# Kernel tuning notes

Measured on AMD Instinct MI355X. Metric: run time of the kernel, lower is better.

## Reference

```python
import jax, jax.numpy as jnp
from jax import lax
import numpy as np

B = 2
N_PER = 12000
TIMES = 16
C_IN = 4
# sparse_shape = grid_size[::-1] + [1,0,0], grid_size=[160,160,40]
S1 = (41, 160, 160)
S2 = (21, 80, 80)   # conv2: k3 s2 p1
S3 = (11, 40, 40)   # conv3: k3 s2 p1
S4 = (5, 20, 20)    # conv4: k3 s2 p(0,1,1)
SOUT = (2, 20, 20)  # conv_out: k(3,1,1) s(2,1,1) p0
# per-BN-layer channel counts, flattened into gamma/beta vectors
CH = [16, 16, 32, 32, 32, 64, 64, 64, 64, 64, 64, 128]
OFF = np.concatenate([[0], np.cumsum(CH)]).tolist()


def _downsample_coords(coords, in_shape, k, s, p):
    # spconv SparseConv3d output index rule: output j active iff some active
    # input x satisfies j*s - p <= x <= j*s - p + k - 1 within bounds.
    out_shape = np.array([(in_shape[i] + 2 * p[i] - k[i]) // s[i] + 1 for i in range(3)])
    b, xs = coords[:, :1], coords[:, 1:]
    s_arr = np.array(s)
    cand = []
    for o0 in range(k[0]):
        for o1 in range(k[1]):
            for o2 in range(k[2]):
                j = xs + np.array([p[0] - o0, p[1] - o1, p[2] - o2])
                ok = np.all(j % s_arr == 0, axis=1)
                jj = j // s_arr
                ok &= np.all((jj >= 0) & (jj < out_shape), axis=1)
                cand.append(np.concatenate([b[ok], jj[ok]], axis=1))
    return np.unique(np.concatenate(cand, axis=0), axis=0).astype(np.int32)


def _make_coords():
    rng = np.random.default_rng(0)
    ncell = S1[0] * S1[1] * S1[2]
    per = []
    for b in range(B):
        flat = rng.choice(ncell, size=N_PER, replace=False)
        z, y, x = np.unravel_index(flat, S1)
        per.append(np.stack([np.full(N_PER, b), z, y, x], axis=1))
    c1 = np.concatenate(per, axis=0).astype(np.int32)
    c2 = _downsample_coords(c1, S1, (3, 3, 3), (2, 2, 2), (1, 1, 1))
    c3 = _downsample_coords(c2, S2, (3, 3, 3), (2, 2, 2), (1, 1, 1))
    c4 = _downsample_coords(c3, S3, (3, 3, 3), (2, 2, 2), (0, 1, 1))
    c5 = _downsample_coords(c4, S4, (3, 1, 1), (2, 1, 1), (0, 0, 0))
    return c1, c2, c3, c4, c5


def _w(key, shape):
    fan_in = shape[0] * shape[1] * shape[2] * shape[3]
    return jax.random.normal(key, shape, jnp.float32) * np.float32(np.sqrt(2.0 / fan_in))


def setup_inputs():
    c1, c2, c3, c4, c5 = _make_coords()
    ks = jax.random.split(jax.random.key(0), 16)
    t = TIMES
    return {
        "voxel_features": jax.random.normal(ks[0], (c1.shape[0], C_IN), jnp.float32),
        "w_in": _w(ks[1], (3, 3, 3, C_IN, t)),
        "w1": _w(ks[2], (3, 3, 3, t, t)),
        "w2_0": _w(ks[3], (3, 3, 3, t, 2 * t)),
        "w2_1": _w(ks[4], (3, 3, 3, 2 * t, 2 * t)),
        "w2_2": _w(ks[5], (3, 3, 3, 2 * t, 2 * t)),
        "w3_0": _w(ks[6], (3, 3, 3, 2 * t, 4 * t)),
        "w3_1": _w(ks[7], (3, 3, 3, 4 * t, 4 * t)),
        "w3_2": _w(ks[8], (3, 3, 3, 4 * t, 4 * t)),
        "w4_0": _w(ks[9], (3, 3, 3, 4 * t, 4 * t)),
        "w4_1": _w(ks[10], (3, 3, 3, 4 * t, 4 * t)),
        "w4_2": _w(ks[11], (3, 3, 3, 4 * t, 4 * t)),
        "w_out": _w(ks[12], (3, 1, 1, 4 * t, 8 * t)),
        "gamma": 1.0 + 0.1 * jax.random.normal(ks[13], (sum(CH),), jnp.float32),
        "beta": 0.1 * jax.random.normal(ks[14], (sum(CH),), jnp.float32),
        "coords1": jnp.asarray(c1), "coords2": jnp.asarray(c2),
        "coords3": jnp.asarray(c3), "coords4": jnp.asarray(c4),
        "coords_out": jnp.asarray(c5),
    }


def _sp_conv(feats, in_coords, w, in_shape, out_coords, stride, padding):
    # spconv's rulebook gather->matmul->scatter over active sites computes the
    # same values as a dense conv on a zero-filled grid, read back only at the
    # active output coordinates (subm: out_coords == in_coords).
    dense = jnp.zeros((B,) + in_shape + (feats.shape[1],), feats.dtype)
    dense = dense.at[in_coords[:, 0], in_coords[:, 1], in_coords[:, 2], in_coords[:, 3]].set(feats)
    out = lax.conv_general_dilated(dense, w, window_strides=stride,
                                   padding=[(p, p) for p in padding],
                                   dimension_numbers=("NDHWC", "DHWIO", "NDHWC"))
    return out[out_coords[:, 0], out_coords[:, 1], out_coords[:, 2], out_coords[:, 3]]


def _bn_relu(x, g, b):
    # nn.BatchNorm1d(eps=1e-3) in training mode over the active voxels, + ReLU
    mu = jnp.mean(x, axis=0)
    var = jnp.mean(jnp.square(x - mu), axis=0)
    return jax.nn.relu((x - mu) * (g * lax.rsqrt(var + 1e-3)) + b)


def _forward(voxel_features, ws, gamma, beta, c1, c2, c3, c4, c5):
    layers = [
        (0, c1, S1, c1, (1, 1, 1), (1, 1, 1)),   # conv_input (subm, 4->16)
        (1, c1, S1, c1, (1, 1, 1), (1, 1, 1)),   # conv1 (subm)
        (2, c1, S1, c2, (2, 2, 2), (1, 1, 1)),   # conv2 spconv s2
        (3, c2, S2, c2, (1, 1, 1), (1, 1, 1)),
        (4, c2, S2, c2, (1, 1, 1), (1, 1, 1)),
        (5, c2, S2, c3, (2, 2, 2), (1, 1, 1)),   # conv3 spconv s2
        (6, c3, S3, c3, (1, 1, 1), (1, 1, 1)),
        (7, c3, S3, c3, (1, 1, 1), (1, 1, 1)),
        (8, c3, S3, c4, (2, 2, 2), (0, 1, 1)),   # conv4 spconv s2, pad (0,1,1)
        (9, c4, S4, c4, (1, 1, 1), (1, 1, 1)),
        (10, c4, S4, c4, (1, 1, 1), (1, 1, 1)),
        (11, c4, S4, c5, (2, 1, 1), (0, 0, 0)),  # conv_out k(3,1,1) s(2,1,1)
    ]
    x = voxel_features
    for i, ci, si, co, st, pd in layers:
        x = _sp_conv(x, ci, ws[i], si, co, st, pd)
        x = _bn_relu(x, gamma[OFF[i]:OFF[i + 1]], beta[OFF[i]:OFF[i + 1]])
    return x  # encoded_spconv_tensor features, [N_out, 8*times]


def reference(voxel_features, w_in, w1, w2_0, w2_1, w2_2, w3_0, w3_1, w3_2,
              w4_0, w4_1, w4_2, w_out, gamma, beta,
              coords1, coords2, coords3, coords4, coords_out):
    ws = [w_in, w1, w2_0, w2_1, w2_2, w3_0, w3_1, w3_2, w4_0, w4_1, w4_2, w_out]
    return _forward(voxel_features, ws, gamma, beta,
                    coords1, coords2, coords3, coords4, coords_out)
```

## Files before the change

### kernel.cpp

```cpp
#include <hip/hip_runtime.h>
#include <hip/hip_bf16.h>


typedef __attribute__((ext_vector_type(8))) short bf16x8;
typedef __attribute__((ext_vector_type(4))) short bf16x4s;
typedef __attribute__((ext_vector_type(4))) float f32x4;

typedef const __attribute__((address_space(1))) unsigned int* gas_ptr;
typedef __attribute__((address_space(3))) unsigned int* las_ptr;

__device__ __forceinline__ void dma16(const unsigned short* g, unsigned short* l) {
    __builtin_amdgcn_global_load_lds((gas_ptr)g, (las_ptr)l, 16, 0, 0);
}

__device__ inline unsigned short f2bf(float f) {
    unsigned u = __builtin_bit_cast(unsigned, f);
    u += 0x7FFFu + ((u >> 16) & 1u);
    return (unsigned short)(u >> 16);
}

struct ScatterArgs {
    const int* coords[4];
    int* grid[4];
    int n[4];
    int D[4], H[4], W[4];
};

__global__ __launch_bounds__(256) void scatter_grid_all(ScatterArgs a) {
    const int l = blockIdx.y;
    const int i = blockIdx.x * 256 + threadIdx.x;
    if (i >= a.n[l]) return;
    const int* c = a.coords[l] + 4 * i;
    a.grid[l][((c[0] * a.D[l] + c[1]) * a.H[l] + c[2]) * a.W[l] + c[3]] = i;
}

struct PrepArgs {
    const float* src[11];
    unsigned short* dst[11];
    int T[11], CIN[11], COUT[11], total[11];
};

__global__ __launch_bounds__(256) void prep_w_all(PrepArgs a) {
    const int l = blockIdx.y;
    const int i = blockIdx.x * 256 + threadIdx.x;
    if (i >= a.total[l]) return;
    const int COUT = a.COUT[l], CIN = a.CIN[l], T = a.T[l];
    const int co = i % COUT; const int r = i / COUT; const int ci = r % CIN; const int t = r / CIN;
    unsigned short v = (t < T) ? f2bf(a.src[l][i]) : (unsigned short)0;
    a.dst[l][((size_t)t * COUT + co) * CIN + ci] = v;
}

__global__ __launch_bounds__(256, 4) void sp_conv0(const float* __restrict__ fin,
                                                   const int* __restrict__ grid,
                                                   const int* __restrict__ oc, int n_out,
                                                   const float* __restrict__ w,
                                                   float* __restrict__ out,
                                                   int D, int H, int W) {
    const int c = threadIdx.x & 15;
    const int p = (blockIdx.x * 256 + threadIdx.x) >> 4;
    if (p >= n_out) return;
    const int b   = oc[4*p+0];
    const int iz0 = oc[4*p+1] - 1;
    const int iy0 = oc[4*p+2] - 1;
    const int ix0 = oc[4*p+3] - 1;
    const int* gb = grid + b * (D * H * W);
    float acc = 0.f;
    for (int kd = 0; kd < 3; ++kd) {
        const int iz = iz0 + kd;
        if ((unsigned)iz >= (unsigned)D) continue;
        for (int kh = 0; kh < 3; ++kh) {
            const int iy = iy0 + kh;
            if ((unsigned)iy >= (unsigned)H) continue;
            for (int kw = 0; kw < 3; ++kw) {
                const int ix = ix0 + kw;
                if ((unsigned)ix >= (unsigned)W) continue;
                const int idx = gb[(iz*H + iy)*W + ix];
                if (idx < 0) continue;
                const float4 v = *(const float4*)(fin + (size_t)idx * 4);
                const float* wp = w + (size_t)((kd*3 + kh)*3 + kw) * 64 + c;
                acc = fmaf(v.x, wp[0],  acc);
                acc = fmaf(v.y, wp[16], acc);
                acc = fmaf(v.z, wp[32], acc);
                acc = fmaf(v.w, wp[48], acc);
            }
        }
    }
    out[(size_t)p*16 + c] = acc;
}

template<int COUT, int BT>
__global__ __launch_bounds__(256, 4) void sp_conv_lds16(
    const unsigned short* __restrict__ fin, const int* __restrict__ grid,
    const int* __restrict__ oc, int n_out,
    const unsigned short* __restrict__ wt, float* __restrict__ out,
    float* __restrict__ stats,
    int D, int H, int W, int sz, int sy, int sx, int pz, int py, int px)
{
    constexpr int T  = 27;
    constexpr int NBATCH = (T + BT - 1)/BT;
    constexpr int TP = NBATCH*BT;
    constexpr int NT = COUT/16;
    constexpr int NB = (COUT == 16) ? BT/2 : BT;

    __shared__ unsigned short Abuf[4*BT*16*16];
    __shared__ unsigned short Bbuf[BT*COUT*16];
    __shared__ float ls[2*COUT];

    const int l     = threadIdx.x & 63;
    const int w     = threadIdx.x >> 6;
    const int n     = l & 15;
    const int quad  = l >> 4;
    const int pbase = blockIdx.x * 64 + w * 16;

    if (threadIdx.x < 2*COUT) ls[threadIdx.x] = 0.f;

    int idx[TP];
    if (quad == 0) {
        int pc = pbase + n;
        if (pc > n_out - 1) pc = n_out - 1;
        const int4 cc = ((const int4*)oc)[pc];
        const int* gb = grid + cc.x * (D * H * W);
        const int iz0 = cc.y * sz - pz;
        const int iy0 = cc.z * sy - py;
        const int ix0 = cc.w * sx - px;
#pragma unroll
        for (int tap = 0; tap < TP; ++tap) {
            const int te = tap < T ? tap : 0;
            const int kd = te/9, kr = te%9, kh = kr/3, kw = kr%3;
            const int iz = iz0 + kd, iy = iy0 + kh, ix = ix0 + kw;
            const bool ok = (tap < T) && (unsigned)iz < (unsigned)D &&
                            (unsigned)iy < (unsigned)H && (unsigned)ix < (unsigned)W;
            const int cz = iz < 0 ? 0 : (iz >= D ? D-1 : iz);
            const int cy = iy < 0 ? 0 : (iy >= H ? H-1 : iy);
            const int cx = ix < 0 ? 0 : (ix >= W ? W-1 : ix);
            const int g = gb[(cz*H + cy)*W + cx];
            idx[tap] = ok ? g : -1;
        }
    }

    f32x4 acc[NT];
#pragma unroll
    for (int t = 0; t < NT; ++t) acc[t] = (f32x4){0.f, 0.f, 0.f, 0.f};

    const int h  = l >> 5;
    const int m  = (l >> 1) & 15;
    const int ch = l & 1;

#pragma unroll
    for (int tb0 = 0; tb0 < TP; tb0 += BT) {
#pragma unroll
        for (int q = 0; q < BT/2; ++q) {
            const int v0 = __shfl(idx[tb0 + 2*q],     m);
            const int v1 = __shfl(idx[tb0 + 2*q + 1], m);
            const int row = h ? v1 : v0;
            const unsigned short* gp = fin + (ptrdiff_t)row*16 + ch*8;
            unsigned short* lp = Abuf + (w*BT + 2*q)*16*16;
            dma16(gp, lp);
        }
        for (int q = w; q < NB; q += 4) {
            if constexpr (COUT == 16) {
                const int tap = tb0 + 2*q + h;
                const int tw = tap < T ? tap : T;
                const unsigned short* gp = wt + ((size_t)tw*COUT + m)*16 + ch*8;
                unsigned short* lp = Bbuf + (2*q)*COUT*16;
                dma16(gp, lp);
            } else {
                const int tap = tb0 + q;
                const int tw = tap < T ? tap : T;
                const int r = l >> 1;
                const unsigned short* gp = wt + ((size_t)tw*COUT + r)*16 + ch*8;
                unsigned short* lp = Bbuf + q*COUT*16;
                dma16(gp, lp);
            }
        }
        __syncthreads();
#pragma unroll
        for (int jp = 0; jp < BT/2; ++jp) {
            const int ts = 2*jp + (quad >> 1);
            bf16x8 a = *(const bf16x8*)(Abuf + ((w*BT + ts)*16 + n)*16 + (quad & 1)*8);
#pragma unroll
            for (int t = 0; t < NT; ++t) {
                bf16x8 b = *(const bf16x8*)(Bbuf + (ts*COUT + t*16 + n)*16 + (quad & 1)*8);
                acc[t] = __builtin_amdgcn_mfma_f32_16x16x32_bf16(a, b, acc[t], 0, 0, 0);
            }
        }
        __syncthreads();
    }

#pragma unroll
    for (int t = 0; t < NT; ++t)
#pragma unroll
        for (int r = 0; r < 4; ++r) {
            const int p = pbase + quad*4 + r;
            if (p < n_out) out[(size_t)p * COUT + t*16 + n] = acc[t][r];
        }

#pragma unroll
    for (int t = 0; t < NT; ++t) {
        float s1 = 0.f, s2 = 0.f;
#pragma unroll
        for (int r = 0; r < 4; ++r) {
            const int p = pbase + quad*4 + r;
            if (p < n_out) { const float v = acc[t][r]; s1 += v; s2 += v*v; }
        }
        s1 += __shfl_xor(s1, 16); s2 += __shfl_xor(s2, 16);
        s1 += __shfl_xor(s1, 32); s2 += __shfl_xor(s2, 32);
        if (quad == 0) {
            atomicAdd(&ls[t*16 + n], s1);
            atomicAdd(&ls[COUT + t*16 + n], s2);
        }
    }
    __syncthreads();
    if (threadIdx.x < 2*COUT) atomicAdd(&stats[threadIdx.x], ls[threadIdx.x]);
}

template<int CIN, int COUT, int BT, int KD, int KH, int KW, int MB>
__global__ __launch_bounds__(256, MB) void sp_conv_lds(
    const unsigned short* __restrict__ fin, const int* __restrict__ grid,
    const int* __restrict__ oc, int n_out,
    const unsigned short* __restrict__ wt, float* __restrict__ out,
    float* __restrict__ stats,
    int D, int H, int W, int sz, int sy, int sx, int pz, int py, int px)
{
    constexpr int T    = KD*KH*KW;
    constexpr int NBATCH = (T + BT - 1)/BT;
    constexpr int TP   = NBATCH*BT;
    constexpr int NT   = COUT/16;
    constexpr int S    = CIN/32;
    constexpr int LPR  = CIN/8;
    constexpr int RPD  = 64/LPR;
    constexpr int ADMA = 16/RPD;
    constexpr int BDMA = COUT/RPD;

    __shared__ unsigned short Abuf[4*BT*16*CIN];
    __shared__ unsigned short Bbuf[BT*COUT*CIN];
    __shared__ float ls[2*COUT];

    const int l     = threadIdx.x & 63;
    const int w     = threadIdx.x >> 6;
    const int n     = l & 15;
    const int quad  = l >> 4;
    const int pbase = blockIdx.x * 64 + w * 16;

    if (threadIdx.x < 2*COUT) ls[threadIdx.x] = 0.f;

    int idx[TP];
    if (quad == 0) {
        int pc = pbase + n;
        if (pc > n_out - 1) pc = n_out - 1;
        const int4 cc = ((const int4*)oc)[pc];
        const int* gb = grid + cc.x * (D * H * W);
        const int iz0 = cc.y * sz - pz;
        const int iy0 = cc.z * sy - py;
        const int ix0 = cc.w * sx - px;
#pragma unroll
        for (int tap = 0; tap < TP; ++tap) {
            const int te = tap < T ? tap : 0;
            const int kd = te/(KH*KW), kr = te%(KH*KW), kh = kr/KW, kw = kr%KW;
            const int iz = iz0 + kd, iy = iy0 + kh, ix = ix0 + kw;
            const bool ok = (tap < T) && (unsigned)iz < (unsigned)D &&
                            (unsigned)iy < (unsigned)H && (unsigned)ix < (unsigned)W;
            const int cz = iz < 0 ? 0 : (iz >= D ? D-1 : iz);
            const int cy = iy < 0 ? 0 : (iy >= H ? H-1 : iy);
            const int cx = ix < 0 ? 0 : (ix >= W ? W-1 : ix);
            const int g = gb[(cz*H + cy)*W + cx];
            idx[tap] = ok ? g : -1;
        }
    }

    f32x4 acc[NT];
#pragma unroll
    for (int t = 0; t < NT; ++t) acc[t] = (f32x4){0.f, 0.f, 0.f, 0.f};

#pragma unroll
    for (int tb0 = 0; tb0 < TP; tb0 += BT) {
#pragma unroll
        for (int j = 0; j < BT; ++j) {
#pragma unroll
            for (int d = 0; d < ADMA; ++d) {
                const int m  = d*RPD + l/LPR;
                const int i0 = __shfl(idx[tb0+j], m);
                const int slot = (l % LPR) ^ (m % LPR);
                const unsigned short* gp = fin + (ptrdiff_t)i0*CIN + slot*8;
                unsigned short* lp = Abuf + ((w*BT + j)*16 + d*RPD)*CIN;
                dma16(gp, lp);
            }
        }
        for (int q = w; q < BT*BDMA; q += 4) {
            const int j = q / BDMA, d = q % BDMA;
            const int t = tb0 + j;
            const int tw = t < T ? t : T;
            const int r  = d*RPD + l/LPR;
            const int slot = (l % LPR) ^ (r % LPR);
            const unsigned short* gp = wt + ((size_t)tw*COUT + r)*CIN + slot*8;
            unsigned short* lp = Bbuf + (j*COUT + d*RPD)*CIN;
            dma16(gp, lp);
        }
        __syncthreads();
#pragma unroll
        for (int j = 0; j < BT; ++j) {
            const unsigned short* Aw = Abuf + (w*BT + j)*16*CIN;
            const unsigned short* Bw = Bbuf + j*COUT*CIN;
#pragma unroll
            for (int s = 0; s < S; ++s) {
                const int c = s*4 + quad;
                bf16x8 a = *(const bf16x8*)(Aw + n*CIN + ((c ^ (n % LPR)) * 8));
#pragma unroll
                for (int t = 0; t < NT; ++t) {
                    const int r = t*16 + n;
                    bf16x8 b = *(const bf16x8*)(Bw + r*CIN + ((c ^ (r % LPR)) * 8));
                    acc[t] = __builtin_amdgcn_mfma_f32_16x16x32_bf16(a, b, acc[t], 0, 0, 0);
                }
            }
        }
        __syncthreads();
    }

#pragma unroll
    for (int t = 0; t < NT; ++t)
#pragma unroll
        for (int r = 0; r < 4; ++r) {
            const int p = pbase + quad*4 + r;
            if (p < n_out) out[(size_t)p * COUT + t*16 + n] = acc[t][r];
        }

#pragma unroll
    for (int t = 0; t < NT; ++t) {
        float s1 = 0.f, s2 = 0.f;
#pragma unroll
        for (int r = 0; r < 4; ++r) {
            const int p = pbase + quad*4 + r;
            if (p < n_out) { const float v = acc[t][r]; s1 += v; s2 += v*v; }
        }
        s1 += __shfl_xor(s1, 16); s2 += __shfl_xor(s2, 16);
        s1 += __shfl_xor(s1, 32); s2 += __shfl_xor(s2, 32);
        if (quad == 0) {
            atomicAdd(&ls[t*16 + n], s1);
            atomicAdd(&ls[COUT + t*16 + n], s2);
        }
    }
    __syncthreads();
    if (threadIdx.x < 2*COUT) atomicAdd(&stats[threadIdx.x], ls[threadIdx.x]);
}

template<int C, int TZ, int TY, int TX, int BTW>
__global__ __launch_bounds__(256, 1) void sp_conv_dense(
    const unsigned short* __restrict__ dense, const int* __restrict__ grid,
    const unsigned short* __restrict__ wt, float* __restrict__ out,
    float* __restrict__ stats, const unsigned short* __restrict__ zrow,
    int D, int H, int W, int ZTn, int YTn, int XTn)
{
    constexpr int T   = 27;
    constexpr int HZ = TZ+2, HY = TY+2, HX = TX+2;
    constexpr int R   = HZ*HY*HX;
    constexpr int LPR = C/8;
    constexpr int RPD = 64/LPR;
    constexpr int RPI = 4*RPD;
    constexpr int NDMA = (R + RPI - 1)/RPI;
    constexpr int RPAD = NDMA*RPI;
    constexpr int M   = TZ*TY*TX;
    constexpr int WPW = M/4;
    constexpr int MT  = WPW/16;
    constexpr int NT  = C/16;
    constexpr int S   = C/32;
    constexpr int BDMA = C/RPD;

    __shared__ unsigned short Hbuf[RPAD*C];
    __shared__ unsigned short Bbuf[BTW*C*C];
    __shared__ float ls[2*C];

    const int l    = threadIdx.x & 63;
    const int w    = threadIdx.x >> 6;
    const int n    = l & 15;
    const int quad = l >> 4;

    int r1 = blockIdx.x;
    const int xt = r1 % XTn; r1 /= XTn;
    const int yt = r1 % YTn; r1 /= YTn;
    const int zt = r1 % ZTn; r1 /= ZTn;
    const int b  = r1;
    const int z0 = zt*TZ, y0 = yt*TY, x0 = xt*TX;
    const int* gb = grid + b * (D*H*W);
    const size_t dbase = (size_t)b * D*H*W;

    if (threadIdx.x < 2*C) ls[threadIdx.x] = 0.f;

#pragma unroll
    for (int d = 0; d < NDMA; ++d) {
        const int r0  = (d*4 + w)*RPD;
        const int row = r0 + l/LPR;
        const int slot = (l % LPR) ^ (row % LPR);
        const unsigned short* gp;
        if (row < R) {
            const int hz = row/(HY*HX);
            const int hy = (row/HX) % HY;
            const int hx = row % HX;
            const int gz = z0 - 1 + hz, gy = y0 - 1 + hy, gx = x0 - 1 + hx;
            const bool ok = (unsigned)gz < (unsigned)D && (unsigned)gy < (unsigned)H &&
                            (unsigned)gx < (unsigned)W;
            gp = ok ? dense + (dbase + (size_t)(gz*H + gy)*W + gx)*C + slot*8
                    : zrow + (l % LPR)*8;
        } else {
            gp = zrow + (l % LPR)*8;
        }
        dma16(gp, Hbuf + r0*C);
    }

    int prow[MT];
#pragma unroll
    for (int mt = 0; mt < MT; ++mt) {
        const int pos = w*WPW + mt*16 + n;
        const int dz = pos/(TY*TX), dy = (pos/TX)%TY, dx = pos%TX;
        prow[mt] = dz*(HY*HX) + dy*HX + dx;
    }

    f32x4 acc[MT][NT];
#pragma unroll
    for (int mt = 0; mt < MT; ++mt)
#pragma unroll
        for (int t = 0; t < NT; ++t) acc[mt][t] = (f32x4){0.f, 0.f, 0.f, 0.f};

#pragma unroll
    for (int batch = 0; batch < (T + BTW - 1)/BTW; ++batch) {
        const int tb0 = batch*BTW;
        const int nb  = (tb0 + BTW <= T) ? BTW : T - tb0;
        for (int q = w; q < nb*BDMA; q += 4) {
            const int j = q / BDMA, d = q % BDMA;
            const int tap = tb0 + j;
            const int rr  = d*RPD + l/LPR;
            const int slot = (l % LPR) ^ (rr % LPR);
            dma16(wt + ((size_t)tap*C + rr)*C + slot*8, Bbuf + (j*C + d*RPD)*C);
        }
        __syncthreads();
#pragma unroll
        for (int j = 0; j < nb; ++j) {
            const int tap = tb0 + j;
            const int kd = tap/9, kh = (tap/3)%3, kw = tap%3;
            const int toff = kd*(HY*HX) + kh*HX + kw;
#pragma unroll
            for (int s = 0; s < S; ++s) {
                const int c = s*4 + quad;
                bf16x8 bfr[NT];
#pragma unroll
                for (int t = 0; t < NT; ++t) {
                    const int rr = t*16 + n;
                    bfr[t] = *(const bf16x8*)(Bbuf + (j*C + rr)*C + ((c ^ (rr & (LPR-1)))*8));
                }
#pragma unroll
                for (int mt = 0; mt < MT; ++mt) {
                    const int arow = prow[mt] + toff;
                    bf16x8 a = *(const bf16x8*)(Hbuf + arow*C + ((c ^ (arow & (LPR-1)))*8));
#pragma unroll
                    for (int t = 0; t < NT; ++t)
                        acc[mt][t] = __builtin_amdgcn_mfma_f32_16x16x32_bf16(a, bfr[t], acc[mt][t], 0, 0, 0);
                }
            }
        }
        __syncthreads();
    }

    float s1[NT], s2[NT];
#pragma unroll
    for (int t = 0; t < NT; ++t) { s1[t] = 0.f; s2[t] = 0.f; }
#pragma unroll
    for (int mt = 0; mt < MT; ++mt) {
#pragma unroll
        for (int r = 0; r < 4; ++r) {
            const int pos = w*WPW + mt*16 + quad*4 + r;
            const int dz = pos/(TY*TX), dy = (pos/TX)%TY, dx = pos%TX;
            const int gz = z0 + dz, gy = y0 + dy, gx = x0 + dx;
            int p = -1;
            if (gz < D && gy < H && gx < W) p = gb[(gz*H + gy)*W + gx];
            if (p >= 0) {
#pragma unroll
                for (int t = 0; t < NT; ++t) {
                    const float v = acc[mt][t][r];
                    out[(size_t)p*C + t*16 + n] = v;
                    s1[t] += v; s2[t] += v*v;
                }
            }
        }
    }
#pragma unroll
    for (int t = 0; t < NT; ++t) {
        float a1 = s1[t], a2 = s2[t];
        a1 += __shfl_xor(a1, 16); a2 += __shfl_xor(a2, 16);
        a1 += __shfl_xor(a1, 32); a2 += __shfl_xor(a2, 32);
        if (quad == 0) {
            atomicAdd(&ls[t*16 + n], a1);
            atomicAdd(&ls[C + t*16 + n], a2);
        }
    }
    __syncthreads();
    if (threadIdx.x < 2*C) atomicAdd(&stats[threadIdx.x], ls[threadIdx.x]);
}

template<int C>
__global__ __launch_bounds__(256) void reduce_stats(const float* __restrict__ x, int nn,
                                                    float* __restrict__ stats)
{
    constexpr int R = 256 / C;
    __shared__ float s1[256];
    __shared__ float s2[256];
    const int c = threadIdx.x % C;
    const int r = threadIdx.x / C;
    float a1 = 0.f, a2 = 0.f;
    for (int i = blockIdx.x * R + r; i < nn; i += R * gridDim.x) {
        float v = x[(size_t)i*C + c];
        a1 += v;
        a2 += v * v;
    }
    s1[threadIdx.x] = a1;
    s2[threadIdx.x] = a2;
    __syncthreads();
    for (int off = 128; off >= C; off >>= 1) {
        if (threadIdx.x < off) {
            s1[threadIdx.x] += s1[threadIdx.x + off];
            s2[threadIdx.x] += s2[threadIdx.x + off];
        }
        __syncthreads();
    }
    if (threadIdx.x < C) {
        atomicAdd(&stats[c],     s1[threadIdx.x]);
        atomicAdd(&stats[C + c], s2[threadIdx.x]);
    }
}

__device__ inline void stv4(float* p, float4 v) { *(float4*)p = v; }
__device__ inline void stv4(unsigned short* p, float4 v) {
    bf16x4s o;
    o.x = (short)f2bf(v.x); o.y = (short)f2bf(v.y);
    o.z = (short)f2bf(v.z); o.w = (short)f2bf(v.w);
    *(bf16x4s*)p = o;
}

__device__ inline float4 bn_math(float4 xv, float4 s1, float4 s2, float4 gm, float4 bt,
                                 float inv_n) {
    float4 o;
    { float mu=s1.x*inv_n, var=s2.x*inv_n-mu*mu, g=gm.x*rsqrtf(var+1e-3f);
      float v=(xv.x-mu)*g+bt.x; o.x = v>0.f? v:0.f; }
    { float mu=s1.y*inv_n, var=s2.y*inv_n-mu*mu, g=gm.y*rsqrtf(var+1e-3f);
      float v=(xv.y-mu)*g+bt.y; o.y = v>0.f? v:0.f; }
    { float mu=s1.z*inv_n, var=s2.z*inv_n-mu*mu, g=gm.z*rsqrtf(var+1e-3f);
      float v=(xv.z-mu)*g+bt.z; o.z = v>0.f? v:0.f; }
    { float mu=s1.w*inv_n, var=s2.w*inv_n-mu*mu, g=gm.w*rsqrtf(var+1e-3f);
      float v=(xv.w-mu)*g+bt.w; o.w = v>0.f? v:0.f; }
    return o;
}

template<int C, typename OUT>
__global__ __launch_bounds__(256) void bn_relu_apply(const float* __restrict__ x,
                                                     OUT* __restrict__ y, int nn,
                                                     const float* __restrict__ stats,
                                                     const float* __restrict__ gamma,
                                                     const float* __restrict__ beta)
{
    const size_t q = (size_t)blockIdx.x * blockDim.x + threadIdx.x;
    if (q >= (size_t)nn * (C/4)) return;
    const int c = (int)(q % (size_t)(C/4)) * 4;
    const float4 o = bn_math(*(const float4*)(x + q*4),
                             *(const float4*)(stats + c), *(const float4*)(stats + C + c),
                             *(const float4*)(gamma + c), *(const float4*)(beta + c),
                             1.f / (float)nn);
    stv4(y + q*4, o);
}

template<int C>
__global__ __launch_bounds__(256) void bn_relu_apply_dense(const float* __restrict__ x,
                                                           unsigned short* __restrict__ dense,
                                                           int nn,
                                                           const float* __restrict__ stats,
                                                           const float* __restrict__ gamma,
                                                           const float* __restrict__ beta,
                                                           const int* __restrict__ coords,
                                                           int D, int H, int W)
{
    const size_t q = (size_t)blockIdx.x * blockDim.x + threadIdx.x;
    if (q >= (size_t)nn * (C/4)) return;
    const int c = (int)(q % (size_t)(C/4)) * 4;
    const int p = (int)(q / (size_t)(C/4));
    const float4 o = bn_math(*(const float4*)(x + q*4),
                             *(const float4*)(stats + c), *(const float4*)(stats + C + c),
                             *(const float4*)(gamma + c), *(const float4*)(beta + c),
                             1.f / (float)nn);
    const int4 cc = ((const int4*)coords)[p];
    const size_t cell = ((size_t)((cc.x*D + cc.y)*H + cc.z)*W + cc.w);
    stv4(dense + cell*C + c, o);
}

extern "C" void kernel_launch(void* const* d_in, const int* in_sizes, int n_in,
                              void* d_out, int out_size, void* d_ws, size_t ws_size,
                              hipStream_t stream) {
    const float* WPTR[12] = {
        (const float*)d_in[1], (const float*)d_in[2], (const float*)d_in[3],
        (const float*)d_in[4], (const float*)d_in[5], (const float*)d_in[6],
        (const float*)d_in[7], (const float*)d_in[8], (const float*)d_in[9],
        (const float*)d_in[10], (const float*)d_in[11], (const float*)d_in[12] };
    const float* vf    = (const float*)d_in[0];
    const float* gamma = (const float*)d_in[13];
    const float* beta  = (const float*)d_in[14];
    const int* c1 = (const int*)d_in[15];
    const int* c2 = (const int*)d_in[16];
    const int* c3 = (const int*)d_in[17];
    const int* c4 = (const int*)d_in[18];
    const int* c5 = (const int*)d_in[19];
    const int N1 = in_sizes[15] / 4;
    const int N2 = in_sizes[16] / 4;
    const int N3 = in_sizes[17] / 4;
    const int N4 = in_sizes[18] / 4;
    const int N5 = in_sizes[19] / 4;

    static const int LT[12]  = {27,27,27,27,27,27,27,27,27,27,27,3};
    static const int LCI[12] = {4,16,16,32,32,32,64,64,64,64,64,64};
    static const int LCO[12] = {16,16,32,32,32,64,64,64,64,64,64,128};

    const size_t G1 = (size_t)2*41*160*160;
    const size_t G2 = (size_t)2*21*80*80;
    const size_t G3 = (size_t)2*11*40*40;
    const size_t G4 = (size_t)2*5*20*20;
    int* grid1 = (int*)d_ws;
    int* grid2 = grid1 + G1;
    int* grid3 = grid2 + G2;
    int* grid4 = grid3 + G3;
    float* stats = (float*)(grid4 + G4);

    size_t maxE = (size_t)N1*16;
    if ((size_t)N2*32  > maxE) maxE = (size_t)N2*32;
    if ((size_t)N3*64  > maxE) maxE = (size_t)N3*64;
    if ((size_t)N4*64  > maxE) maxE = (size_t)N4*64;
    if ((size_t)N5*128 > maxE) maxE = (size_t)N5*128;
    maxE = (maxE + 7) & ~(size_t)7;

    float* raw = stats + 12*256;
    unsigned short* padA = (unsigned short*)(raw + maxE);
    unsigned short* fA   = padA + 128;
    unsigned short* padB = fA + maxE;
    unsigned short* fB   = padB + 128;
    unsigned short* wtb  = fB + maxE;
    size_t wtoff[12];
    size_t wtot = 0;
    {
        size_t o = 0;
        for (int i = 1; i < 12; ++i) {
            wtoff[i] = o;
            o += (size_t)(LT[i] + 1) * LCI[i] * LCO[i];
        }
        wtot = (o + 15) & ~(size_t)15;
    }
    unsigned short* dbuf = wtb + wtot;

    hipMemsetAsync(grid1, 0xFF, (G1+G2+G3+G4)*sizeof(int), stream);
    hipMemsetAsync(stats, 0, 12*256*sizeof(float), stream);
    hipMemsetAsync(padA, 0, 128*sizeof(unsigned short), stream);
    hipMemsetAsync(padB, 0, 128*sizeof(unsigned short), stream);

    {
        ScatterArgs sa;
        sa.coords[0]=c1; sa.coords[1]=c2; sa.coords[2]=c3; sa.coords[3]=c4;
        sa.grid[0]=grid1; sa.grid[1]=grid2; sa.grid[2]=grid3; sa.grid[3]=grid4;
        sa.n[0]=N1; sa.n[1]=N2; sa.n[2]=N3; sa.n[3]=N4;
        sa.D[0]=41; sa.H[0]=160; sa.W[0]=160;
        sa.D[1]=21; sa.H[1]= 80; sa.W[1]= 80;
        sa.D[2]=11; sa.H[2]= 40; sa.W[2]= 40;
        sa.D[3]= 5; sa.H[3]= 20; sa.W[3]= 20;
        int mx = N1; if (N2>mx) mx=N2; if (N3>mx) mx=N3; if (N4>mx) mx=N4;
        dim3 g((mx + 255)/256, 4);
        scatter_grid_all<<<g, 256, 0, stream>>>(sa);
    }
    {
        PrepArgs pa;
        int mx = 0;
        for (int i = 1; i < 12; ++i) {
            pa.src[i-1] = WPTR[i];
            pa.dst[i-1] = wtb + wtoff[i];
            pa.T[i-1] = LT[i]; pa.CIN[i-1] = LCI[i]; pa.COUT[i-1] = LCO[i];
            pa.total[i-1] = (LT[i]+1)*LCI[i]*LCO[i];
            if (pa.total[i-1] > mx) mx = pa.total[i-1];
        }
        dim3 g((mx + 255)/256, 11);
        prep_w_all<<<g, 256, 0, stream>>>(pa);
    }

    enum { GOFF_0 = 0, GOFF_1 = 16, GOFF_2 = 32, GOFF_3 = 64, GOFF_4 = 96, GOFF_5 = 128,
           GOFF_6 = 192, GOFF_7 = 256, GOFF_8 = 320, GOFF_9 = 384, GOFF_10 = 448, GOFF_11 = 512 };

#define APPLY(i, COUT, NP, FOUT_T, FOUT) \
    bn_relu_apply<COUT, FOUT_T><<<(((size_t)(NP)*(COUT)/4) + 255)/256, 256, 0, stream>>>( \
        raw, FOUT, NP, stats + (i)*256, gamma + GOFF_##i, beta + GOFF_##i);

#define APPLYD(i, C, NP, CC, D,H,W) \
    hipMemsetAsync(dbuf, 0, (size_t)2*(D)*(H)*(W)*(C)*2, stream); \
    bn_relu_apply_dense<C><<<(((size_t)(NP)*(C)/4) + 255)/256, 256, 0, stream>>>( \
        raw, dbuf, NP, stats + (i)*256, gamma + GOFF_##i, beta + GOFF_##i, CC, D,H,W);

    sp_conv0<<<((size_t)N1*16 + 255)/256, 256, 0, stream>>>(vf, grid1, c1, N1, WPTR[0], raw, 41,160,160);
    { int rb = (N1 + 15)/16; if (rb > 240) rb = 240;
      reduce_stats<16><<<rb, 256, 0, stream>>>(raw, N1, stats + 0*256); }
    APPLY(0, 16, N1, unsigned short, fA);

#define CONVS(i, COUT, BT, FIN, GRD, OC, NP, D,H,W, SZ,SY,SX, PZ,PY,PX) \
    sp_conv_lds16<COUT,BT><<<((NP)+63)/64, 256, 0, stream>>>( \
        FIN, GRD, OC, NP, wtb + wtoff[i], raw, stats + (i)*256, D,H,W, SZ,SY,SX, PZ,PY,PX);

#define CONVL(i, CIN, COUT, BT, MB, KD,KH,KW, FIN, GRD, OC, NP, D,H,W, SZ,SY,SX, PZ,PY,PX) \
    sp_conv_lds<CIN,COUT,BT,KD,KH,KW,MB><<<((NP)+63)/64, 256, 0, stream>>>( \
        FIN, GRD, OC, NP, wtb + wtoff[i], raw, stats + (i)*256, D,H,W, SZ,SY,SX, PZ,PY,PX);

#define CONVD(i, C, TZ,TY,TX, BTW, GRD, D,H,W) \
    { const int zt = ((D)+(TZ)-1)/(TZ), yt = ((H)+(TY)-1)/(TY), xt = ((W)+(TX)-1)/(TX); \
      sp_conv_dense<C,TZ,TY,TX,BTW><<<2*zt*yt*xt, 256, 0, stream>>>( \
          dbuf, GRD, wtb + wtoff[i], raw, stats + (i)*256, padA, D,H,W, zt,yt,xt); }

    CONVS( 1, 16, 10,   fA, grid1, c1, N1, 41,160,160, 1,1,1, 1,1,1); APPLY( 1, 16, N1, unsigned short, fB);
    CONVS( 2, 32, 10,   fB, grid1, c2, N2, 41,160,160, 2,2,2, 1,1,1); APPLYD( 2, 32, N2, c2, 21,80,80);
    CONVD( 3, 32, 4,8,16, 27, grid2, 21,80,80);                       APPLYD( 3, 32, N2, c2, 21,80,80);
    CONVD( 4, 32, 4,8,16, 27, grid2, 21,80,80);                       APPLY( 4, 32, N2, unsigned short, fA);
    CONVL( 5, 32, 64, 9, 2, 3,3,3, fA, grid2, c3, N3, 21,80,80, 2,2,2, 1,1,1); APPLYD( 5, 64, N3, c3, 11,40,40);
    CONVD( 6, 64, 4,4,8, 10, grid3, 11,40,40);                        APPLYD( 6, 64, N3, c3, 11,40,40);
    CONVD( 7, 64, 4,4,8, 10, grid3, 11,40,40);                        APPLY( 7, 64, N3, unsigned short, fB);
    CONVL( 8, 64, 64, 9, 1, 3,3,3, fB, grid3, c4, N4, 11,40,40, 2,2,2, 0,1,1); APPLYD( 8, 64, N4, c4, 5,20,20);
    CONVD( 9, 64, 4,4,8, 10, grid4, 5,20,20);                         APPLYD( 9, 64, N4, c4, 5,20,20);
    CONVD(10, 64, 4,4,8, 10, grid4, 5,20,20);                         APPLY(10, 64, N4, unsigned short, fA);
    CONVL(11, 64,128, 3, 2, 3,1,1, fA, grid4, c5, N5,  5,20,20, 2,1,1, 0,0,0); APPLY(11, 128, N5, float, (float*)d_out);
#undef CONVS
#undef CONVL
#undef CONVD
#undef APPLY
#undef APPLYD
}
```

Baseline: 462.7 us.

## Replace dense convs at levels 2 and 4 with gather MFMA kernels, add XCD swizzle

Adds an sp_conv_big gather kernel that computes 32 output rows per wave (two M tiles), so each weight fragment feeds more MFMAs. Layers 3 and 4 now use it instead of the dense-grid conv, and layers 9 and 10 use the sparse gather kernel, which removes the dense scatter and memset at those levels. It also adds an XCD-aware remap of block indices, fixes the lds16 tap batch size at 4, and changes the dense kernel's batch and occupancy settings. The risk is more register pressure and whether gather beats dense at the 80x80 density.

```diff
diff --git a/kernel.cpp b/kernel.cpp
--- a/kernel.cpp
+++ b/kernel.cpp
@@ -11,6 +11,12 @@
 
 __device__ __forceinline__ void dma16(const unsigned short* g, unsigned short* l) {
     __builtin_amdgcn_global_load_lds((gas_ptr)g, (las_ptr)l, 16, 0, 0);
+}
+
+__device__ __forceinline__ int xcd_swz(int wg, int nwg) {
+    const int x = wg & 7, i = wg >> 3;
+    const int q = nwg >> 3, r = nwg & 7;
+    return (x < r ? x * (q + 1) : r * (q + 1) + (x - r) * q) + i;
 }
 
 __device__ inline unsigned short f2bf(float f) {
@@ -88,7 +94,7 @@
     out[(size_t)p*16 + c] = acc;
 }
 
-template<int COUT, int BT>
+template<int COUT>
 __global__ __launch_bounds__(256, 4) void sp_conv_lds16(
     const unsigned short* __restrict__ fin, const int* __restrict__ grid,
     const int* __restrict__ oc, int n_out,
@@ -97,8 +103,8 @@
     int D, int H, int W, int sz, int sy, int sx, int pz, int py, int px)
 {
     constexpr int T  = 27;
-    constexpr int NBATCH = (T + BT - 1)/BT;
-    constexpr int TP = NBATCH*BT;
+    constexpr int BT = 4;
+    constexpr int TP = 28;
     constexpr int NT = COUT/16;
     constexpr int NB = (COUT == 16) ? BT/2 : BT;
 
@@ -110,7 +116,7 @@
     const int w     = threadIdx.x >> 6;
     const int n     = l & 15;
     const int quad  = l >> 4;
-    const int pbase = blockIdx.x * 64 + w * 16;
+    const int pbase = xcd_swz(blockIdx.x, gridDim.x) * 64 + w * 16;
 
     if (threadIdx.x < 2*COUT) ls[threadIdx.x] = 0.f;
 
@@ -223,8 +229,7 @@
     int D, int H, int W, int sz, int sy, int sx, int pz, int py, int px)
 {
     constexpr int T    = KD*KH*KW;
-    constexpr int NBATCH = (T + BT - 1)/BT;
-    constexpr int TP   = NBATCH*BT;
+    constexpr int TP   = ((T + BT - 1)/BT)*BT;
     constexpr int NT   = COUT/16;
     constexpr int S    = CIN/32;
     constexpr int LPR  = CIN/8;
@@ -240,7 +245,7 @@
     const int w     = threadIdx.x >> 6;
     const int n     = l & 15;
     const int quad  = l >> 4;
-    const int pbase = blockIdx.x * 64 + w * 16;
+    const int pbase = xcd_swz(blockIdx.x, gridDim.x) * 64 + w * 16;
 
     if (threadIdx.x < 2*COUT) ls[threadIdx.x] = 0.f;
 
@@ -343,8 +348,149 @@
     if (threadIdx.x < 2*COUT) atomicAdd(&stats[threadIdx.x], ls[threadIdx.x]);
 }
 
-template<int C, int TZ, int TY, int TX, int BTW>
-__global__ __launch_bounds__(256, 1) void sp_conv_dense(
+template<int CIN, int COUT, int BT, int MB>
+__global__ __launch_bounds__(256, MB) void sp_conv_big(
+    const unsigned short* __restrict__ fin, const int* __restrict__ grid,
+    const int* __restrict__ oc, int n_out,
+    const unsigned short* __restrict__ wt, float* __restrict__ out,
+    float* __restrict__ stats,
+    int D, int H, int W, int sz, int sy, int sx, int pz, int py, int px)
+{
+    constexpr int T    = 27;
+    constexpr int TP   = 28;
+    constexpr int MT   = 2;
+    constexpr int NT   = COUT/16;
+    constexpr int S    = CIN/32;
+    constexpr int LPR  = CIN/8;
+    constexpr int RPD  = 64/LPR;
+    constexpr int ADMA = 32/RPD;
+    constexpr int BDMA = COUT/RPD;
+
+    __shared__ unsigned short Abuf[4*BT*32*CIN];
+    __shared__ unsigned short Bbuf[BT*COUT*CIN];
+    __shared__ float ls[2*COUT];
+
+    const int l     = threadIdx.x & 63;
+    const int w     = threadIdx.x >> 6;
+    const int n     = l & 15;
+    const int quad  = l >> 4;
+    const int wbase = xcd_swz(blockIdx.x, gridDim.x) * 128 + w * 32;
+
+    if (threadIdx.x < 2*COUT) ls[threadIdx.x] = 0.f;
+
+    int idx[TP];
+    {
+        int pc = wbase + (l & 31);
+        if (pc > n_out - 1) pc = n_out - 1;
+        const int4 cc = ((const int4*)oc)[pc];
+        const int* gb = grid + cc.x * (D * H * W);
+        const int iz0 = cc.y * sz - pz;
+        const int iy0 = cc.z * sy - py;
+        const int ix0 = cc.w * sx - px;
+#pragma unroll
+        for (int tap = 0; tap < TP; ++tap) {
+            const int te = tap < T ? tap : 0;
+            const int kd = te/9, kr = te%9, kh = kr/3, kw = kr%3;
+            const int iz = iz0 + kd, iy = iy0 + kh, ix = ix0 + kw;
+            const bool ok = (tap < T) && (unsigned)iz < (unsigned)D &&
+                            (unsigned)iy < (unsigned)H && (unsigned)ix < (unsigned)W;
+            const int cz = iz < 0 ? 0 : (iz >= D ? D-1 : iz);
+            const int cy = iy < 0 ? 0 : (iy >= H ? H-1 : iy);
+            const int cx = ix < 0 ? 0 : (ix >= W ? W-1 : ix);
+            const int g = gb[(cz*H + cy)*W + cx];
+            idx[tap] = ok ? g : -1;
+        }
+    }
+
+    f32x4 acc[MT][NT];
+#pragma unroll
+    for (int mt = 0; mt < MT; ++mt)
+#pragma unroll
+        for (int t = 0; t < NT; ++t) acc[mt][t] = (f32x4){0.f, 0.f, 0.f, 0.f};
+
+#pragma unroll
+    for (int tb0 = 0; tb0 < TP; tb0 += BT) {
+#pragma unroll
+        for (int j = 0; j < BT; ++j) {
+#pragma unroll
+            for (int d = 0; d < ADMA; ++d) {
+                const int r  = d*RPD + l/LPR;
+                const int i0 = __shfl(idx[tb0+j], r);
+                const int slot = (l % LPR) ^ (r % LPR);
+                const unsigned short* gp = fin + (ptrdiff_t)i0*CIN + slot*8;
+                unsigned short* lp = Abuf + ((w*BT + j)*32 + d*RPD)*CIN;
+                dma16(gp, lp);
+            }
+        }
+        for (int q = w; q < BT*BDMA; q += 4) {
+            const int j = q / BDMA, d = q % BDMA;
+            const int t = tb0 + j;
+            const int tw = t < T ? t : T;
+            const int r  = d*RPD + l/LPR;
+            const int slot = (l % LPR) ^ (r % LPR);
+            const unsigned short* gp = wt + ((size_t)tw*COUT + r)*CIN + slot*8;
+            unsigned short* lp = Bbuf + (j*COUT + d*RPD)*CIN;
+            dma16(gp, lp);
+        }
+        __syncthreads();
+#pragma unroll
+        for (int j = 0; j < BT; ++j) {
+            const unsigned short* Aw = Abuf + (w*BT + j)*32*CIN;
+            const unsigned short* Bw = Bbuf + j*COUT*CIN;
+#pragma unroll
+            for (int s = 0; s < S; ++s) {
+                const int c = s*4 + quad;
+                bf16x8 bfr[NT];
+#pragma unroll
+                for (int t = 0; t < NT; ++t) {
+                    const int r = t*16 + n;
+                    bfr[t] = *(const bf16x8*)(Bw + r*CIN + ((c ^ (r % LPR)) * 8));
+                }
+#pragma unroll
+                for (int mt = 0; mt < MT; ++mt) {
+                    bf16x8 a = *(const bf16x8*)(Aw + (mt*16 + n)*CIN + ((c ^ (n % LPR)) * 8));
+#pragma unroll
+                    for (int t = 0; t < NT; ++t)
+                        acc[mt][t] = __builtin_amdgcn_mfma_f32_16x16x32_bf16(a, bfr[t], acc[mt][t], 0, 0, 0);
+                }
+            }
+        }
+        __syncthreads();
+    }
+
+#pragma unroll
+    for (int mt = 0; mt < MT; ++mt)
+#pragma unroll
+        for (int t = 0; t < NT; ++t)
+#pragma unroll
+            for (int r = 0; r < 4; ++r) {
+                const int p = wbase + mt*16 + quad*4 + r;
+                if (p < n_out) out[(size_t)p * COUT + t*16 + n] = acc[mt][t][r];
+            }
+
+#pragma unroll
+    for (int t = 0; t < NT; ++t) {
+        float s1 = 0.f, s2 = 0.f;
+#pragma unroll
+        for (int mt = 0; mt < MT; ++mt)
+#pragma unroll
+            for (int r = 0; r < 4; ++r) {
+                const int p = wbase + mt*16 + quad*4 + r;
+                if (p < n_out) { const float v = acc[mt][t][r]; s1 += v; s2 += v*v; }
+            }
+        s1 += __shfl_xor(s1, 16); s2 += __shfl_xor(s2, 16);
+        s1 += __shfl_xor(s1, 32); s2 += __shfl_xor(s2, 32);
+        if (quad == 0) {
+            atomicAdd(&ls[t*16 + n], s1);
+            atomicAdd(&ls[COUT + t*16 + n], s2);
+        }
+    }
+    __syncthreads();
+    if (threadIdx.x < 2*COUT) atomicAdd(&stats[threadIdx.x], ls[threadIdx.x]);
+}
+
+template<int C, int TZ, int TY, int TX, int BTW, int MB>
+__global__ __launch_bounds__(256, MB) void sp_conv_dense(
     const unsigned short* __restrict__ dense, const int* __restrict__ grid,
     const unsigned short* __restrict__ wt, float* __restrict__ out,
     float* __restrict__ stats, const unsigned short* __restrict__ zrow,
@@ -698,32 +844,37 @@
       reduce_stats<16><<<rb, 256, 0, stream>>>(raw, N1, stats + 0*256); }
     APPLY(0, 16, N1, unsigned short, fA);
 
-#define CONVS(i, COUT, BT, FIN, GRD, OC, NP, D,H,W, SZ,SY,SX, PZ,PY,PX) \
-    sp_conv_lds16<COUT,BT><<<((NP)+63)/64, 256, 0, stream>>>( \
+#define CONVS(i, COUT, FIN, GRD, OC, NP, D,H,W, SZ,SY,SX, PZ,PY,PX) \
+    sp_conv_lds16<COUT><<<((NP)+63)/64, 256, 0, stream>>>( \
         FIN, GRD, OC, NP, wtb + wtoff[i], raw, stats + (i)*256, D,H,W, SZ,SY,SX, PZ,PY,PX);
 
 #define CONVL(i, CIN, COUT, BT, MB, KD,KH,KW, FIN, GRD, OC, NP, D,H,W, SZ,SY,SX, PZ,PY,PX) \
     sp_conv_lds<CIN,COUT,BT,KD,KH,KW,MB><<<((NP)+63)/64, 256, 0, stream>>>( \
         FIN, GRD, OC, NP, wtb + wtoff[i], raw, stats + (i)*256, D,H,W, SZ,SY,SX, PZ,PY,PX);
 
-#define CONVD(i, C, TZ,TY,TX, BTW, GRD, D,H,W) \
+#define CONVB(i, CIN, COUT, BT, MB, FIN, GRD, OC, NP, D,H,W, SZ,SY,SX, PZ,PY,PX) \
+    sp_conv_big<CIN,COUT,BT,MB><<<((NP)+127)/128, 256, 0, stream>>>( \
+        FIN, GRD, OC, NP, wtb + wtoff[i], raw, stats + (i)*256, D,H,W, SZ,SY,SX, PZ,PY,PX);
+
+#define CONVD(i, C, TZ,TY,TX, BTW, MB, GRD, D,H,W) \
     { const int zt = ((D)+(TZ)-1)/(TZ), yt = ((H)+(TY)-1)/(TY), xt = ((W)+(TX)-1)/(TX); \
-      sp_conv_dense<C,TZ,TY,TX,BTW><<<2*zt*yt*xt, 256, 0, stream>>>( \
+      sp_conv_dense<C,TZ,TY,TX,BTW,MB><<<2*zt*yt*xt, 256, 0, stream>>>( \
           dbuf, GRD, wtb + wtoff[i], raw, stats + (i)*256, padA, D,H,W, zt,yt,xt); }
 
-    CONVS( 1, 16, 10,   fA, grid1, c1, N1, 41,160,160, 1,1,1, 1,1,1); APPLY( 1, 16, N1, unsigned short, fB);
-    CONVS( 2, 32, 10,   fB, grid1, c2, N2, 41,160,160, 2,2,2, 1,1,1); APPLYD( 2, 32, N2, c2, 21,80,80);
-    CONVD( 3, 32, 4,8,16, 27, grid2, 21,80,80);                       APPLYD( 3, 32, N2, c2, 21,80,80);
-    CONVD( 4, 32, 4,8,16, 27, grid2, 21,80,80);                       APPLY( 4, 32, N2, unsigned short, fA);
-    CONVL( 5, 32, 64, 9, 2, 3,3,3, fA, grid2, c3, N3, 21,80,80, 2,2,2, 1,1,1); APPLYD( 5, 64, N3, c3, 11,40,40);
-    CONVD( 6, 64, 4,4,8, 10, grid3, 11,40,40);                        APPLYD( 6, 64, N3, c3, 11,40,40);
-    CONVD( 7, 64, 4,4,8, 10, grid3, 11,40,40);                        APPLY( 7, 64, N3, unsigned short, fB);
-    CONVL( 8, 64, 64, 9, 1, 3,3,3, fB, grid3, c4, N4, 11,40,40, 2,2,2, 0,1,1); APPLYD( 8, 64, N4, c4, 5,20,20);
-    CONVD( 9, 64, 4,4,8, 10, grid4, 5,20,20);                         APPLYD( 9, 64, N4, c4, 5,20,20);
-    CONVD(10, 64, 4,4,8, 10, grid4, 5,20,20);                         APPLY(10, 64, N4, unsigned short, fA);
-    CONVL(11, 64,128, 3, 2, 3,1,1, fA, grid4, c5, N5,  5,20,20, 2,1,1, 0,0,0); APPLY(11, 128, N5, float, (float*)d_out);
+    CONVS( 1, 16,       fA, grid1, c1, N1, 41,160,160, 1,1,1, 1,1,1); APPLY( 1, 16, N1, unsigned short, fB);
+    CONVS( 2, 32,       fB, grid1, c2, N2, 41,160,160, 2,2,2, 1,1,1); APPLY( 2, 32, N2, unsigned short, fA);
+    CONVB ( 3, 32, 32, 7, 2, fA, grid2, c2, N2, 21, 80, 80, 1,1,1, 1,1,1); APPLY( 3, 32, N2, unsigned short, fB);
+    CONVB ( 4, 32, 32, 7, 2, fB, grid2, c2, N2, 21, 80, 80, 1,1,1, 1,1,1); APPLY( 4, 32, N2, unsigned short, fA);
+    CONVB ( 5, 32, 64, 4, 3, fA, grid2, c3, N3, 21, 80, 80, 2,2,2, 1,1,1); APPLYD( 5, 64, N3, c3, 11,40,40);
+    CONVD ( 6, 64, 4,4,8, 3, 2, grid3, 11,40,40);                          APPLYD( 6, 64, N3, c3, 11,40,40);
+    CONVD ( 7, 64, 4,4,8, 3, 2, grid3, 11,40,40);                          APPLY( 7, 64, N3, unsigned short, fB);
+    CONVL ( 8, 64, 64, 9, 1, 3,3,3, fB, grid3, c4, N4, 11, 40, 40, 2,2,2, 0,1,1); APPLY( 8, 64, N4, unsigned short, fA);
+    CONVL ( 9, 64, 64, 9, 1, 3,3,3, fA, grid4, c4, N4,  5, 20, 20, 1,1,1, 1,1,1); APPLY( 9, 64, N4, unsigned short, fB);
+    CONVL (10, 64, 64, 9, 1, 3,3,3, fB, grid4, c4, N4,  5, 20, 20, 1,1,1, 1,1,1); APPLY(10, 64, N4, unsigned short, fA);
+    CONVL (11, 64,128, 3, 2, 3,1,1, fA, grid4, c5, N5,  5, 20, 20, 2,1,1, 0,0,0); APPLY(11, 128, N5, float, (float*)d_out);
 #undef CONVS
 #undef CONVL
+#undef CONVB
 #undef CONVD
 #undef APPLY
 #undef APPLYD
```

New measurement: 388.7 us. 1.19x faster.
